# Kernel optimization log

Measured on AMD Instinct MI355X. Metric: run time of the kernel, lower is better.

## Reference

```python
import jax, jax.numpy as jnp
import numpy as np
from jax import lax

GAMMA = 0.99

def setup_inputs() -> dict:
    key = jax.random.key(0)
    ks = jax.random.split(key, 6)
    B, T, D = 2048, 512, 16
    return {
        "Q": jax.random.normal(ks[0], (B, T, D), dtype=jnp.float32),
        "expected_target_Q": jax.random.normal(ks[1], (B, T, D), dtype=jnp.float32),
        "target_Q": jax.random.normal(ks[2], (B, T, D), dtype=jnp.float32),
        "rewards": jax.random.normal(ks[3], (B, T, D), dtype=jnp.float32),
        "target_policy_probs": jax.random.normal(ks[4], (B, T, D), dtype=jnp.float32),
        "behaviour_policy_probs": jax.random.normal(ks[5], (B, T), dtype=jnp.float32),
    }


def _q_ret(expected_target_Q, target_Q, rewards, target_policy_probs, behaviour_policy_probs):
    # importance weights c = exp(min(log_pi - log_b, 0)), shape [B, T, D]
    c = jnp.exp(jnp.minimum(target_policy_probs - behaviour_policy_probs[..., None], 0.0))
    T = target_Q.shape[1]
    # time-major slices for steps j = 0..T-2
    tm = lambda x: jnp.swapaxes(x, 0, 1)  # [T, B, D] -> scan over leading axis
    xs = (tm(rewards[:, : T - 1]), tm(expected_target_Q[:, 1:]),
          tm(c[:, 1:]), tm(target_Q[:, 1:]))

    def step(carry, x):
        r, e, cw, tq = x
        q = r + GAMMA * (e + cw * (carry - tq))
        return q, q

    # reverse scan: Q_ret[j] depends on Q_ret[j+1]; init carry is target_Q[:, -1]
    _, q_ret = lax.scan(step, target_Q[:, -1], xs, reverse=True)
    return jnp.swapaxes(q_ret, 0, 1)  # [B, T-1, D] == Q_ret[:, :-1]


def reference(Q, expected_target_Q, target_Q, rewards, target_policy_probs, behaviour_policy_probs):
    q_ret = lax.stop_gradient(
        _q_ret(expected_target_Q, target_Q, rewards, target_policy_probs, behaviour_policy_probs))
    return jnp.mean((Q[:, :-1] - q_ret) ** 2)
```

## Files before the change

kernel.cpp:

```cpp
#include <hip/hip_runtime.h>


constexpr int B = 2048;
constexpr int T = 512;
constexpr int D = 16;
constexpr int NC = 16;
constexpr int CS = 32;
constexpr int SQ = B * (D / 4);
constexpr float GAMMA = 0.99f;
constexpr float LOG2E = 1.44269504088896340736f;

__global__ __launch_bounds__(256) void retrace_phase1(
    const float* __restrict__ Q,
    const float* __restrict__ eQ,
    const float* __restrict__ tQ,
    const float* __restrict__ rw,
    const float* __restrict__ tpp,
    const float* __restrict__ bpp,
    float4* __restrict__ ws)
{
    const int s  = blockIdx.x * blockDim.x + threadIdx.x;
    const int k  = blockIdx.y;
    const int b  = s >> 2;
    const int dq = s & 3;

    const int j_start = k * CS;
    const int j_end   = min(j_start + CS, T - 1);

    const float4* __restrict__ q4 = (const float4*)Q;
    const float4* __restrict__ e4 = (const float4*)eQ;
    const float4* __restrict__ t4 = (const float4*)tQ;
    const float4* __restrict__ r4 = (const float4*)rw;
    const float4* __restrict__ p4 = (const float4*)tpp;
    const size_t row = (size_t)b * T * 4 + dq;
    const float* __restrict__ b_p = bpp + (size_t)b * T;

    float alpha[4] = {0.f, 0.f, 0.f, 0.f};
    float beta[4]  = {1.f, 1.f, 1.f, 1.f};
    float P[4] = {0.f, 0.f, 0.f, 0.f};
    float S[4] = {0.f, 0.f, 0.f, 0.f};
    float W[4] = {0.f, 0.f, 0.f, 0.f};

    #pragma unroll 4
    for (int j = j_end - 1; j >= j_start; --j) {
        const float4 tp4 = p4[row + (size_t)(j + 1) * 4];
        const float4 tq4 = t4[row + (size_t)(j + 1) * 4];
        const float4 ee4 = e4[row + (size_t)(j + 1) * 4];
        const float4 rr4 = r4[row + (size_t)j * 4];
        const float4 qq4 = q4[row + (size_t)j * 4];
        const float  bp  = b_p[j + 1];

        const float* tp = (const float*)&tp4;
        const float* tq = (const float*)&tq4;
        const float* ee = (const float*)&ee4;
        const float* rr = (const float*)&rr4;
        const float* qq = (const float*)&qq4;

        #pragma unroll
        for (int i = 0; i < 4; ++i) {
            const float cw = __builtin_exp2f(fminf(tp[i] - bp, 0.f) * LOG2E);
            const float g  = GAMMA * cw;
            const float base = fmaf(-g, tq[i], fmaf(GAMMA, ee[i], rr[i]));
            alpha[i] = fmaf(g, alpha[i], base);
            beta[i]  = g * beta[i];
            const float u = qq[i] - alpha[i];
            P[i] = fmaf(u, u, P[i]);
            S[i] = fmaf(u, beta[i], S[i]);
            W[i] = fmaf(beta[i], beta[i], W[i]);
        }
    }

    const size_t o = (size_t)k * SQ + s;
    float4* wsA = ws;
    float4* wsM = ws + (size_t)NC * SQ;
    float4* wsP = ws + (size_t)2 * NC * SQ;
    float4* wsS = ws + (size_t)3 * NC * SQ;
    float4* wsW = ws + (size_t)4 * NC * SQ;
    wsA[o] = *(const float4*)alpha;
    wsM[o] = *(const float4*)beta;
    wsP[o] = *(const float4*)P;
    wsS[o] = *(const float4*)S;
    wsW[o] = *(const float4*)W;
}

__global__ __launch_bounds__(64) void retrace_phase2(
    const float* __restrict__ tQ,
    const float4* __restrict__ ws,
    float* __restrict__ out)
{
    const int s  = blockIdx.x * blockDim.x + threadIdx.x;
    const int b  = s >> 2;
    const int dq = s & 3;

    const float4* wsA = ws;
    const float4* wsM = ws + (size_t)NC * SQ;
    const float4* wsP = ws + (size_t)2 * NC * SQ;
    const float4* wsS = ws + (size_t)3 * NC * SQ;
    const float4* wsW = ws + (size_t)4 * NC * SQ;

    float4 c4 = ((const float4*)tQ)[((size_t)b * T + (T - 1)) * 4 + dq];
    float* c = (float*)&c4;
    float loss[4] = {0.f, 0.f, 0.f, 0.f};

    for (int k = NC - 1; k >= 0; --k) {
        const size_t o = (size_t)k * SQ + s;
        const float4 A4 = wsA[o], M4 = wsM[o], P4 = wsP[o], S4 = wsS[o], W4 = wsW[o];
        const float* A = (const float*)&A4;
        const float* M = (const float*)&M4;
        const float* P = (const float*)&P4;
        const float* S = (const float*)&S4;
        const float* W = (const float*)&W4;
        #pragma unroll
        for (int i = 0; i < 4; ++i) {
            loss[i] += fmaf(c[i], fmaf(W[i], c[i], -2.f * S[i]), P[i]);
            c[i] = fmaf(M[i], c[i], A[i]);
        }
    }

    float acc = (loss[0] + loss[1]) + (loss[2] + loss[3]);
    #pragma unroll
    for (int off = 32; off > 0; off >>= 1)
        acc += __shfl_down(acc, off, 64);

    if (threadIdx.x == 0) {
        constexpr float inv_count = 1.0f / ((float)B * (float)(T - 1) * (float)D);
        atomicAdd(out, acc * inv_count);
    }
}

extern "C" void kernel_launch(void* const* d_in, const int* in_sizes, int n_in,
                              void* d_out, int out_size, void* d_ws, size_t ws_size,
                              hipStream_t stream) {
    const float* Q   = (const float*)d_in[0];
    const float* eQ  = (const float*)d_in[1];
    const float* tQ  = (const float*)d_in[2];
    const float* rw  = (const float*)d_in[3];
    const float* tpp = (const float*)d_in[4];
    const float* bpp = (const float*)d_in[5];
    float* out = (float*)d_out;
    float4* ws = (float4*)d_ws;

    hipMemsetAsync(out, 0, sizeof(float), stream);

    retrace_phase1<<<dim3(SQ / 256, NC), dim3(256), 0, stream>>>(
        Q, eQ, tQ, rw, tpp, bpp, ws);

    retrace_phase2<<<dim3(SQ / 64), dim3(64), 0, stream>>>(tQ, ws, out);
}
```

Measured before the change: 320.0 us.

## Stage phase-1 chunks in LDS via direct global-to-LDS loads, one thread per feature

Phase 1 now gives each 64-thread block four batch rows and one time chunk. It copies the contiguous chunk of all five inputs into shared memory with buffer-to-LDS loads, then runs the backward recurrence with one thread per feature dimension, reading from LDS. Before, each thread walked time with large strides and loaded 64-byte pieces per row, which coalesced poorly; the new layout makes global reads fully contiguous. In exchange, shared-memory use per block is large, which caps occupancy, and there is no overlap between the load phase and the compute phase. Phase 2's chunk loop is also fully unrolled.

```diff
diff --git a/kernel.cpp b/kernel.cpp
--- a/kernel.cpp
+++ b/kernel.cpp
@@ -1,86 +1,110 @@
 #include <hip/hip_runtime.h>
 
 
-constexpr int B = 2048;
-constexpr int T = 512;
-constexpr int D = 16;
+constexpr int B  = 2048;
+constexpr int T  = 512;
+constexpr int D  = 16;
 constexpr int NC = 16;
 constexpr int CS = 32;
+constexpr int BPB = 4;
+constexpr int ROWS = CS + 1;
 constexpr int SQ = B * (D / 4);
 constexpr float GAMMA = 0.99f;
 constexpr float LOG2E = 1.44269504088896340736f;
 
-__global__ __launch_bounds__(256) void retrace_phase1(
+constexpr int SEG = ROWS * D;
+constexpr int ARR = BPB * SEG;
+constexpr int LDS_FLOATS = 5 * ARR + BPB * ROWS;
+
+__device__ __forceinline__ void load_lds16(const float* g, float* l) {
+    __builtin_amdgcn_global_load_lds(
+        (const __attribute__((address_space(1))) unsigned int*)g,
+        (__attribute__((address_space(3))) unsigned int*)l, 16, 0, 0);
+}
+__device__ __forceinline__ void load_lds4(const float* g, float* l) {
+    __builtin_amdgcn_global_load_lds(
+        (const __attribute__((address_space(1))) unsigned int*)g,
+        (__attribute__((address_space(3))) unsigned int*)l, 4, 0, 0);
+}
+
+__global__ __launch_bounds__(64) void retrace_phase1(
     const float* __restrict__ Q,
     const float* __restrict__ eQ,
     const float* __restrict__ tQ,
     const float* __restrict__ rw,
     const float* __restrict__ tpp,
     const float* __restrict__ bpp,
-    float4* __restrict__ ws)
+    float* __restrict__ ws)
 {
-    const int s  = blockIdx.x * blockDim.x + threadIdx.x;
-    const int k  = blockIdx.y;
-    const int b  = s >> 2;
-    const int dq = s & 3;
+    __shared__ float lds[LDS_FLOATS];
 
-    const int j_start = k * CS;
-    const int j_end   = min(j_start + CS, T - 1);
+    const int tid = threadIdx.x;
+    const int k   = blockIdx.y;
+    const int b0  = blockIdx.x * BPB;
+    const int t0  = k * CS;
 
-    const float4* __restrict__ q4 = (const float4*)Q;
-    const float4* __restrict__ e4 = (const float4*)eQ;
-    const float4* __restrict__ t4 = (const float4*)tQ;
-    const float4* __restrict__ r4 = (const float4*)rw;
-    const float4* __restrict__ p4 = (const float4*)tpp;
-    const size_t row = (size_t)b * T * 4 + dq;
-    const float* __restrict__ b_p = bpp + (size_t)b * T;
+    const bool last = (k == NC - 1);
+    const int rows = last ? CS : ROWS;
+    const int n4   = rows * D / 4;
 
-    float alpha[4] = {0.f, 0.f, 0.f, 0.f};
-    float beta[4]  = {1.f, 1.f, 1.f, 1.f};
-    float P[4] = {0.f, 0.f, 0.f, 0.f};
-    float S[4] = {0.f, 0.f, 0.f, 0.f};
-    float W[4] = {0.f, 0.f, 0.f, 0.f};
-
-    #pragma unroll 4
-    for (int j = j_end - 1; j >= j_start; --j) {
-        const float4 tp4 = p4[row + (size_t)(j + 1) * 4];
-        const float4 tq4 = t4[row + (size_t)(j + 1) * 4];
-        const float4 ee4 = e4[row + (size_t)(j + 1) * 4];
-        const float4 rr4 = r4[row + (size_t)j * 4];
-        const float4 qq4 = q4[row + (size_t)j * 4];
-        const float  bp  = b_p[j + 1];
-
-        const float* tp = (const float*)&tp4;
-        const float* tq = (const float*)&tq4;
-        const float* ee = (const float*)&ee4;
-        const float* rr = (const float*)&rr4;
-        const float* qq = (const float*)&qq4;
-
+    const float* gbase[5] = {Q, eQ, tQ, rw, tpp};
+    #pragma unroll
+    for (int a = 0; a < 5; ++a) {
         #pragma unroll
-        for (int i = 0; i < 4; ++i) {
-            const float cw = __builtin_exp2f(fminf(tp[i] - bp, 0.f) * LOG2E);
-            const float g  = GAMMA * cw;
-            const float base = fmaf(-g, tq[i], fmaf(GAMMA, ee[i], rr[i]));
-            alpha[i] = fmaf(g, alpha[i], base);
-            beta[i]  = g * beta[i];
-            const float u = qq[i] - alpha[i];
-            P[i] = fmaf(u, u, P[i]);
-            S[i] = fmaf(u, beta[i], S[i]);
-            W[i] = fmaf(beta[i], beta[i], W[i]);
+        for (int bl = 0; bl < BPB; ++bl) {
+            const float* g = gbase[a] + ((size_t)(b0 + bl) * T + t0) * D;
+            float* l = lds + a * ARR + bl * SEG;
+            for (int off = tid; off < n4; off += 64)
+                load_lds16(g + (size_t)off * 4, l + (size_t)off * 4);
         }
     }
+    #pragma unroll
+    for (int bl = 0; bl < BPB; ++bl) {
+        const float* g = bpp + (size_t)(b0 + bl) * T + t0;
+        float* l = lds + 5 * ARR + bl * ROWS;
+        if (tid < rows) load_lds4(g + tid, l + tid);
+    }
+    __syncthreads();
 
-    const size_t o = (size_t)k * SQ + s;
-    float4* wsA = ws;
-    float4* wsM = ws + (size_t)NC * SQ;
-    float4* wsP = ws + (size_t)2 * NC * SQ;
-    float4* wsS = ws + (size_t)3 * NC * SQ;
-    float4* wsW = ws + (size_t)4 * NC * SQ;
-    wsA[o] = *(const float4*)alpha;
-    wsM[o] = *(const float4*)beta;
-    wsP[o] = *(const float4*)P;
-    wsS[o] = *(const float4*)S;
-    wsW[o] = *(const float4*)W;
+    const int bl = tid >> 4;
+    const int d  = tid & 15;
+    const float* lQ = lds + 0 * ARR + bl * SEG + d;
+    const float* lE = lds + 1 * ARR + bl * SEG + d;
+    const float* lT = lds + 2 * ARR + bl * SEG + d;
+    const float* lR = lds + 3 * ARR + bl * SEG + d;
+    const float* lP = lds + 4 * ARR + bl * SEG + d;
+    const float* lB = lds + 5 * ARR + bl * ROWS;
+
+    const int steps = last ? (CS - 1) : CS;
+
+    float alpha = 0.f, beta = 1.f, P = 0.f, S = 0.f, W = 0.f;
+    #pragma unroll 8
+    for (int i = steps - 1; i >= 0; --i) {
+        const float tp = lP[(i + 1) * D];
+        const float tq = lT[(i + 1) * D];
+        const float ev = lE[(i + 1) * D];
+        const float rv = lR[i * D];
+        const float qv = lQ[i * D];
+        const float bp = lB[i + 1];
+
+        const float cw = __builtin_exp2f(fminf(tp - bp, 0.f) * LOG2E);
+        const float g  = GAMMA * cw;
+        const float base = fmaf(-g, tq, fmaf(GAMMA, ev, rv));
+        alpha = fmaf(g, alpha, base);
+        beta  = g * beta;
+        const float u = qv - alpha;
+        P = fmaf(u, u, P);
+        S = fmaf(u, beta, S);
+        W = fmaf(beta, beta, W);
+    }
+
+    const size_t AS = (size_t)NC * SQ * 4;
+    const size_t o  = ((size_t)k * SQ + (size_t)b0 * 4) * 4 + tid;
+    ws[0 * AS + o] = alpha;
+    ws[1 * AS + o] = beta;
+    ws[2 * AS + o] = P;
+    ws[3 * AS + o] = S;
+    ws[4 * AS + o] = W;
 }
 
 __global__ __launch_bounds__(64) void retrace_phase2(
@@ -102,6 +126,7 @@
     float* c = (float*)&c4;
     float loss[4] = {0.f, 0.f, 0.f, 0.f};
 
+    #pragma unroll
     for (int k = NC - 1; k >= 0; --k) {
         const size_t o = (size_t)k * SQ + s;
         const float4 A4 = wsA[o], M4 = wsM[o], P4 = wsP[o], S4 = wsS[o], W4 = wsW[o];
@@ -138,12 +163,12 @@
     const float* tpp = (const float*)d_in[4];
     const float* bpp = (const float*)d_in[5];
     float* out = (float*)d_out;
-    float4* ws = (float4*)d_ws;
+    float* ws = (float*)d_ws;
 
     hipMemsetAsync(out, 0, sizeof(float), stream);
 
-    retrace_phase1<<<dim3(SQ / 256, NC), dim3(256), 0, stream>>>(
+    retrace_phase1<<<dim3(B / BPB, NC), dim3(64), 0, stream>>>(
         Q, eQ, tQ, rw, tpp, bpp, ws);
 
-    retrace_phase2<<<dim3(SQ / 64), dim3(64), 0, stream>>>(tQ, ws, out);
+    retrace_phase2<<<dim3(SQ / 64), dim3(64), 0, stream>>>(tQ, (const float4*)ws, out);
 }
```

After: 305.5 us. 4.5% less time.
